# Optimization experiments

Measured on AMD Instinct MI355X. Metric: run time of the kernel, lower is better.

The kernel has to match this reference:

```python
import jax, jax.numpy as jnp
import numpy as np

N_HEADS = 4
N_HIDDEN = 512  # out_features with concat=False
SLOPE = 0.01
NEG = -1e9


def setup_inputs() -> dict:
    key = jax.random.key(0)
    k1, k2, k3, k4 = jax.random.split(key, 4)
    N, F_IN = 8192, 512
    h = jax.random.normal(k1, (N, F_IN), dtype=jnp.float32)
    W = jax.random.normal(k2, (F_IN, N_HIDDEN * N_HEADS), dtype=jnp.float32) * 0.05
    a = jax.random.normal(k3, (N_HEADS, 2 * N_HIDDEN, 1), dtype=jnp.float32) * 0.05
    adj_mat = jnp.where(jax.random.uniform(k4, (N, N)) < 0.01, 0.0, NEG).astype(jnp.float32)
    return {"h": h, "adj_mat": adj_mat, "W": W, "a": a}


def reference(h, adj_mat, W, a):
    N = h.shape[0]
    # [N, H*d] -> [H, N, d]
    ht = (h @ W).reshape(N, N_HEADS, N_HIDDEN).transpose(1, 0, 2)
    a_src = a[:, :N_HIDDEN, 0]   # [H, d]
    a_dst = a[:, N_HIDDEN:, 0]   # [H, d]
    src = jnp.einsum('hnd,hd->hn', ht, a_src)  # [H, N]
    dst = jnp.einsum('hnd,hd->hn', ht, a_dst)  # [H, N]
    # e[h,i,j] = leaky_relu(src[h,i] + dst[h,j]) + adj_mat[i,j]
    e = jax.nn.leaky_relu(src[:, :, None] + dst[:, None, :], SLOPE) + adj_mat[None]
    att = jax.nn.softmax(e, axis=-1)           # [H, N, N]
    h_prime = jnp.einsum('hij,hjd->hid', att, ht)  # [H, N, d]
    return h_prime.mean(axis=0)                # concat=False -> head mean, [N, d]
```

## Files before the change

### kernel.cpp

```cpp
#include <hip/hip_runtime.h>
#include <stdint.h>

#define NN 8192
#define DH 512
#define NH 4
#define LOG2E 1.4426950408889634f

typedef __attribute__((ext_vector_type(8))) short short8;
typedef __attribute__((ext_vector_type(4))) float f32x4;

__device__ __forceinline__ unsigned short f2bf(float f) {
    unsigned int u = __float_as_uint(f);
    unsigned int r = (u + 0x7fffu + ((u >> 16) & 1u)) >> 16;
    return (unsigned short)r;
}
__device__ __forceinline__ float bf2f(unsigned short s) {
    return __uint_as_float(((unsigned int)s) << 16);
}

__device__ __forceinline__ void global_to_lds16(const void* g, void* l) {
    __builtin_amdgcn_global_load_lds(
        (const __attribute__((address_space(1))) unsigned int*)g,
        (__attribute__((address_space(3))) unsigned int*)l, 16, 0, 0);
}

__global__ void k_convert_h(const float* __restrict__ hf, unsigned short* __restrict__ hb) {
    const int idx = (blockIdx.x * 256 + threadIdx.x) * 8;
    const float4 f0 = *(const float4*)(hf + idx);
    const float4 f1 = *(const float4*)(hf + idx + 4);
    uint4 o;
    o.x = (unsigned)f2bf(f0.x) | ((unsigned)f2bf(f0.y) << 16);
    o.y = (unsigned)f2bf(f0.z) | ((unsigned)f2bf(f0.w) << 16);
    o.z = (unsigned)f2bf(f1.x) | ((unsigned)f2bf(f1.y) << 16);
    o.w = (unsigned)f2bf(f1.z) | ((unsigned)f2bf(f1.w) << 16);
    *(uint4*)(hb + idx) = o;
}

__global__ void k_transpose_W(const float* __restrict__ W, unsigned short* __restrict__ Wt) {
    __shared__ float t[32][33];
    const int tx = threadIdx.x & 31, ty = threadIdx.x >> 5;
    const int p0 = blockIdx.x * 32, k0 = blockIdx.y * 32;
#pragma unroll
    for (int r = 0; r < 4; r++)
        t[ty + r * 8][tx] = W[(k0 + ty + r * 8) * 2048 + p0 + tx];
    __syncthreads();
#pragma unroll
    for (int r = 0; r < 4; r++)
        Wt[(size_t)(p0 + ty + r * 8) * 512 + k0 + tx] = f2bf(t[tx][ty + r * 8]);
}

__global__ __launch_bounds__(256, 3) void k_gemm(const unsigned short* __restrict__ Wt,
                                                 const unsigned short* __restrict__ hb,
                                                 unsigned short* __restrict__ vt) {
    __shared__ alignas(16) char smem[32768];
    const int tid = threadIdx.x;
    const int w = tid >> 6, lane = tid & 63;
    const int lr = lane & 15, lc = lane >> 4;
    const int pBase = blockIdx.y * 128, nBase = blockIdx.x * 128;
    f32x4 acc[4][4] = {};
    const int wr = (w >> 1) * 64, wc = (w & 1) * 64;
    for (int kb = 0; kb < 8; kb++) {
        const int k0 = kb * 64;
#pragma unroll
        for (int it = 0; it < 4; it++) {
            const int o = it * 4096 + w * 1024 + lane * 16;
            const int row = o >> 7;
            const int koff = (o & 127) >> 1;
            global_to_lds16(Wt + (size_t)(pBase + row) * 512 + k0 + koff,
                            smem + it * 4096 + w * 1024);
            global_to_lds16(hb + (size_t)(nBase + row) * 512 + k0 + koff,
                            smem + 16384 + it * 4096 + w * 1024);
        }
        __syncthreads();
#pragma unroll
        for (int kk = 0; kk < 2; kk++) {
            short8 a[4], b[4];
#pragma unroll
            for (int m = 0; m < 4; m++)
                a[m] = *(const short8*)(smem + (wr + m * 16 + lr) * 128 + kk * 64 + lc * 16);
#pragma unroll
            for (int n = 0; n < 4; n++)
                b[n] = *(const short8*)(smem + 16384 + (wc + n * 16 + lr) * 128 + kk * 64 + lc * 16);
#pragma unroll
            for (int m = 0; m < 4; m++)
#pragma unroll
                for (int n = 0; n < 4; n++)
                    acc[m][n] = __builtin_amdgcn_mfma_f32_16x16x32_bf16(a[m], b[n], acc[m][n], 0, 0, 0);
        }
        __syncthreads();
    }
#pragma unroll
    for (int m = 0; m < 4; m++)
#pragma unroll
        for (int n = 0; n < 4; n++)
#pragma unroll
            for (int q = 0; q < 4; q++) {
                const int p = pBase + wr + m * 16 + lc * 4 + q;
                const int ncol = nBase + wc + n * 16 + lr;
                vt[(size_t)p * NN + ncol] = f2bf(acc[m][n][q]);
            }
}

__global__ void k_srcdst(const unsigned short* __restrict__ vt, const float* __restrict__ a,
                         float* __restrict__ srcL, float* __restrict__ dstL) {
    const int n = blockIdx.x * 256 + threadIdx.x;
    const int h = blockIdx.y;
    const int d0 = blockIdx.z * 64;
    float s = 0.f, t = 0.f;
#pragma unroll 4
    for (int d = d0; d < d0 + 64; d++) {
        const float v = bf2f(vt[(size_t)(h * 512 + d) * NN + n]);
        s += v * a[h * 1024 + d];
        t += v * a[h * 1024 + 512 + d];
    }
    __hip_atomic_fetch_add(&srcL[h * NN + n], s * LOG2E, __ATOMIC_RELAXED, __HIP_MEMORY_SCOPE_AGENT);
    __hip_atomic_fetch_add(&dstL[h * NN + n], t * LOG2E, __ATOMIC_RELAXED, __HIP_MEMORY_SCOPE_AGENT);
}

#define VB(b) (smem + (b) * 32768)
#define PB(b) (smem + 65536 + (b) * 8192)
#define D_OFF 81920
#define NJT (NN / 32)
__global__ __launch_bounds__(512, 2) void k_flash(const float* __restrict__ adj,
                                                  const unsigned short* __restrict__ vt,
                                                  const float* __restrict__ srcL,
                                                  const float* __restrict__ dstL,
                                                  float* __restrict__ out) {
    __shared__ alignas(16) char smem[82432];
    const int tid = threadIdx.x;
    const int w = tid >> 6, lane = tid & 63;
    const int lr = lane & 15, lc = lane >> 4;
    const int h = blockIdx.x & 3;
    const int i0 = (int)(blockIdx.x >> 2) * 128;
    const int ih = w >> 2, dq = w & 3;
    float* denom = (float*)(smem + D_OFF);

    const int srow = i0 + w * 16 + lr;
    const float srcv = srcL[h * NN + srow];
    const float* __restrict__ adjrow = adj + (size_t)srow * NN;
    const float* __restrict__ dstLh = dstL + h * NN;
    const unsigned short* __restrict__ vth = vt + (size_t)(h * 512) * NN;
    float dsum = 0.f;
    f32x4 acc[4][8] = {};

    const int prow = w * 16 + lr;
    const int psl = (((prow & 1) << 2) | lc) ^ ((prow >> 1) & 7);
    const int poff = (prow >> 1) * 128 + (psl << 4);

#define STAGE(J0, BUF)                                                                   \
    {                                                                                    \
        _Pragma("unroll") for (int it = 0; it < 4; it++) {                               \
            const int o = it * 8192 + w * 1024 + lane * 16;                              \
            const int row = o >> 7;                                                      \
            const int z = ((o >> 4) & 7) ^ (row & 7);                                    \
            const int d = (row << 1) | (z >> 2);                                         \
            const int j = (J0) + ((z & 3) << 3);                                         \
            global_to_lds16(vth + (size_t)d * NN + j, VB(BUF) + it * 8192 + w * 1024);   \
        }                                                                                \
    }

#define LOADROW(J0)                                                                      \
    {                                                                                    \
        const int jc8 = (J0) + lc * 8;                                                   \
        aj0 = *(const float4*)(adjrow + jc8);                                            \
        aj1 = *(const float4*)(adjrow + jc8 + 4);                                        \
        dl0 = *(const float4*)(dstLh + jc8);                                             \
        dl1 = *(const float4*)(dstLh + jc8 + 4);                                         \
    }

#define SCORE()                                                                          \
    {                                                                                    \
        const float padj[8] = {aj0.x, aj0.y, aj0.z, aj0.w, aj1.x, aj1.y, aj1.z, aj1.w};  \
        const float pdst[8] = {dl0.x, dl0.y, dl0.z, dl0.w, dl1.x, dl1.y, dl1.z, dl1.w};  \
        _Pragma("unroll") for (int q = 0; q < 8; q++) {                                  \
            const float x = srcv + pdst[q];                                              \
            const float l2 = fmaxf(x, 0.01f * x);                                        \
            const float p = exp2f(l2 + padj[q]);                                         \
            dsum += p;                                                                   \
            pfrag[q] = (short)f2bf(p);                                                   \
        }                                                                                \
    }

#define PV(BUF)                                                                          \
    {                                                                                    \
        const char* vb = VB(BUF);                                                        \
        const char* pb = PB(BUF);                                                        \
        short8 afr[4];                                                                   \
        _Pragma("unroll") for (int t = 0; t < 4; t++) {                                  \
            const int rr = ih * 64 + t * 16 + lr;                                        \
            const int sl = (((rr & 1) << 2) | lc) ^ ((rr >> 1) & 7);                     \
            afr[t] = *(const short8*)(pb + (rr >> 1) * 128 + (sl << 4));                 \
        }                                                                                \
        __builtin_amdgcn_s_setprio(1);                                                   \
        _Pragma("unroll") for (int s = 0; s < 8; s++) {                                  \
            const int d = dq * 128 + s * 16 + lr;                                        \
            const int sl = (((d & 1) << 2) | lc) ^ ((d >> 1) & 7);                       \
            const short8 bfr = *(const short8*)(vb + (d >> 1) * 128 + (sl << 4));        \
            _Pragma("unroll") for (int t = 0; t < 4; t++)                                \
                acc[t][s] = __builtin_amdgcn_mfma_f32_16x16x32_bf16(afr[t], bfr,         \
                                                                    acc[t][s], 0, 0, 0); \
        }                                                                                \
        __builtin_amdgcn_s_setprio(0);                                                   \
    }

    float4 aj0, aj1, dl0, dl1;
    short8 pfrag;
    LOADROW(0);
    STAGE(0, 0);
    SCORE();
    *(short8*)(PB(0) + poff) = pfrag;
    __syncthreads();
#pragma unroll 1
    for (int jb = 0; jb < NJT - 1; jb++) {
        const int cur = jb & 1, nxt = cur ^ 1;
        LOADROW((jb + 1) * 32);
        STAGE((jb + 1) * 32, nxt);
        PV(cur);
        SCORE();
        *(short8*)(PB(nxt) + poff) = pfrag;
        __syncthreads();
    }
    PV((NJT - 1) & 1);

    dsum += __shfl_xor(dsum, 16, 64);
    dsum += __shfl_xor(dsum, 32, 64);
    if (lane < 16) denom[w * 16 + lane] = dsum;
    __syncthreads();
#pragma unroll
    for (int t = 0; t < 4; t++) {
        const int rl = ih * 64 + t * 16 + lc * 4;
#pragma unroll
        for (int q = 0; q < 4; q++) {
            const float inv = 0.25f / denom[rl + q];
            float* orow = out + (size_t)(i0 + rl + q) * 512;
#pragma unroll
            for (int s = 0; s < 8; s++) {
                const int d = dq * 128 + s * 16 + lr;
                __hip_atomic_fetch_add(orow + d, acc[t][s][q] * inv,
                                       __ATOMIC_RELAXED, __HIP_MEMORY_SCOPE_AGENT);
            }
        }
    }
}

extern "C" void kernel_launch(void* const* d_in, const int* in_sizes, int n_in,
                              void* d_out, int out_size, void* d_ws, size_t ws_size,
                              hipStream_t stream) {
    const float* h = (const float*)d_in[0];
    const float* adj = (const float*)d_in[1];
    const float* W = (const float*)d_in[2];
    const float* a = (const float*)d_in[3];
    float* out = (float*)d_out;
    char* ws = (char*)d_ws;
    unsigned short* hb = (unsigned short*)ws;
    unsigned short* Wt = (unsigned short*)(ws + 8388608);
    unsigned short* vt = (unsigned short*)(ws + 8388608 + 2097152);
    float* srcL = (float*)(ws + 8388608 + 2097152 + 33554432);
    float* dstL = srcL + NH * NN;

    hipMemsetAsync(d_out, 0, (size_t)out_size * sizeof(float), stream);
    hipMemsetAsync(srcL, 0, 2 * NH * NN * sizeof(float), stream);
    k_convert_h<<<2048, 256, 0, stream>>>(h, hb);
    k_transpose_W<<<dim3(64, 16), 256, 0, stream>>>(W, Wt);
    k_gemm<<<dim3(64, 16), 256, 0, stream>>>(Wt, hb, vt);
    k_srcdst<<<dim3(32, NH, 8), 256, 0, stream>>>(vt, a, srcL, dstL);
    k_flash<<<256, 512, 0, stream>>>(adj, vt, srcL, dstL, out);
}
```

Baseline: 874.8 us.

## Triple-buffer V tiles with partial vmcnt wait and raw barrier in flash loop

Moves the V staging from a double buffer to a rotating triple buffer in LDS. Each iteration now waits only for the previous tile's async global-to-LDS loads (vmcnt(8)) before a raw s_barrier, so the next tile's loads stay in flight across the barrier instead of being drained by __syncthreads. It also precomputes the per-thread V gather offsets and the adj/dst row pointers once, outside the loop. In exchange, LDS use per block grows from about 82 KB to about 115 KB, which may stop two 512-thread blocks from sharing a CU and so cut occupancy.

```diff
diff --git a/kernel.cpp b/kernel.cpp
--- a/kernel.cpp
+++ b/kernel.cpp
@@ -117,16 +117,14 @@
     __hip_atomic_fetch_add(&dstL[h * NN + n], t * LOG2E, __ATOMIC_RELAXED, __HIP_MEMORY_SCOPE_AGENT);
 }
 
-#define VB(b) (smem + (b) * 32768)
-#define PB(b) (smem + 65536 + (b) * 8192)
-#define D_OFF 81920
+#define D_OFF 114688
 #define NJT (NN / 32)
 __global__ __launch_bounds__(512, 2) void k_flash(const float* __restrict__ adj,
                                                   const unsigned short* __restrict__ vt,
                                                   const float* __restrict__ srcL,
                                                   const float* __restrict__ dstL,
                                                   float* __restrict__ out) {
-    __shared__ alignas(16) char smem[82432];
+    __shared__ alignas(16) char smem[115200];
     const int tid = threadIdx.x;
     const int w = tid >> 6, lane = tid & 63;
     const int lr = lane & 15, lc = lane >> 4;
@@ -137,35 +135,43 @@
 
     const int srow = i0 + w * 16 + lr;
     const float srcv = srcL[h * NN + srow];
-    const float* __restrict__ adjrow = adj + (size_t)srow * NN;
-    const float* __restrict__ dstLh = dstL + h * NN;
+    const float* __restrict__ adjp = adj + (size_t)srow * NN + lc * 8;
+    const float* __restrict__ dlp = dstL + h * NN + lc * 8;
     const unsigned short* __restrict__ vth = vt + (size_t)(h * 512) * NN;
     float dsum = 0.f;
     f32x4 acc[4][8] = {};
 
+    unsigned voff[4];
+#pragma unroll
+    for (int it = 0; it < 4; it++) {
+        const int o = it * 8192 + w * 1024 + lane * 16;
+        const int row = o >> 7;
+        const int z = ((o >> 4) & 7) ^ (row & 7);
+        const int d = (row << 1) | (z >> 2);
+        voff[it] = (unsigned)d * NN + ((z & 3) << 3);
+    }
     const int prow = w * 16 + lr;
     const int psl = (((prow & 1) << 2) | lc) ^ ((prow >> 1) & 7);
     const int poff = (prow >> 1) * 128 + (psl << 4);
 
-#define STAGE(J0, BUF)                                                                   \
-    {                                                                                    \
-        _Pragma("unroll") for (int it = 0; it < 4; it++) {                               \
-            const int o = it * 8192 + w * 1024 + lane * 16;                              \
-            const int row = o >> 7;                                                      \
-            const int z = ((o >> 4) & 7) ^ (row & 7);                                    \
-            const int d = (row << 1) | (z >> 2);                                         \
-            const int j = (J0) + ((z & 3) << 3);                                         \
-            global_to_lds16(vth + (size_t)d * NN + j, VB(BUF) + it * 8192 + w * 1024);   \
-        }                                                                                \
+    char* vc = smem;
+    char* vn = smem + 32768;
+    char* vnn = smem + 65536;
+    char* pc = smem + 98304;
+    char* pn = smem + 106496;
+
+#define STAGE(J0, DST)                                                                   \
+    {                                                                                    \
+        _Pragma("unroll") for (int it = 0; it < 4; it++)                                 \
+            global_to_lds16(vth + voff[it] + (J0), (DST) + it * 8192 + w * 1024);        \
     }
 
 #define LOADROW(J0)                                                                      \
     {                                                                                    \
-        const int jc8 = (J0) + lc * 8;                                                   \
-        aj0 = *(const float4*)(adjrow + jc8);                                            \
-        aj1 = *(const float4*)(adjrow + jc8 + 4);                                        \
-        dl0 = *(const float4*)(dstLh + jc8);                                             \
-        dl1 = *(const float4*)(dstLh + jc8 + 4);                                         \
+        aj0 = *(const float4*)(adjp + (J0));                                             \
+        aj1 = *(const float4*)(adjp + (J0) + 4);                                         \
+        dl0 = *(const float4*)(dlp + (J0));                                              \
+        dl1 = *(const float4*)(dlp + (J0) + 4);                                          \
     }
 
 #define SCORE()                                                                          \
@@ -181,10 +187,10 @@
         }                                                                                \
     }
 
-#define PV(BUF)                                                                          \
-    {                                                                                    \
-        const char* vb = VB(BUF);                                                        \
-        const char* pb = PB(BUF);                                                        \
+#define PV(VBUF, PBUF)                                                                   \
+    {                                                                                    \
+        const char* vb = (VBUF);                                                         \
+        const char* pb = (PBUF);                                                         \
         short8 afr[4];                                                                   \
         _Pragma("unroll") for (int t = 0; t < 4; t++) {                                  \
             const int rr = ih * 64 + t * 16 + lr;                                        \
@@ -206,21 +212,29 @@
     float4 aj0, aj1, dl0, dl1;
     short8 pfrag;
     LOADROW(0);
-    STAGE(0, 0);
+    STAGE(0, vc);
     SCORE();
-    *(short8*)(PB(0) + poff) = pfrag;
-    __syncthreads();
+    *(short8*)(pc + poff) = pfrag;
 #pragma unroll 1
     for (int jb = 0; jb < NJT - 1; jb++) {
-        const int cur = jb & 1, nxt = cur ^ 1;
-        LOADROW((jb + 1) * 32);
-        STAGE((jb + 1) * 32, nxt);
-        PV(cur);
+        const int J0 = (jb + 1) * 32;
+        LOADROW(J0);
+        STAGE(J0, vn);
+        asm volatile("s_waitcnt vmcnt(8) lgkmcnt(0)" ::: "memory");
+        __builtin_amdgcn_sched_barrier(0);
+        __builtin_amdgcn_s_barrier();
+        __builtin_amdgcn_sched_barrier(0);
+        PV(vc, pc);
         SCORE();
-        *(short8*)(PB(nxt) + poff) = pfrag;
-        __syncthreads();
-    }
-    PV((NJT - 1) & 1);
+        *(short8*)(pn + poff) = pfrag;
+        char* tv = vc; vc = vn; vn = vnn; vnn = tv;
+        char* tp = pc; pc = pn; pn = tp;
+    }
+    asm volatile("s_waitcnt vmcnt(0) lgkmcnt(0)" ::: "memory");
+    __builtin_amdgcn_sched_barrier(0);
+    __builtin_amdgcn_s_barrier();
+    __builtin_amdgcn_sched_barrier(0);
+    PV(vc, pc);
 
     dsum += __shfl_xor(dsum, 16, 64);
     dsum += __shfl_xor(dsum, 32, 64);
```

New measurement: 808.8 us. 1.08x faster.
